# Kernel tuning notes

Hardware: AMD Instinct MI355X
Metric: run time of the kernel (lower is better)

Reference implementation:

```python
import jax, jax.numpy as jnp
import numpy as np

SEED_THRESHOLD = 0.5
DUPLICATE_THRESHOLD = 0.8


def setup_inputs() -> dict:
    key = jax.random.key(0)
    k1, k2 = jax.random.split(key)
    B, Q, C = 16, 1800, 256
    return {
        "query_signatures": jax.random.normal(k1, (B, Q, C), dtype=jnp.float32),
        "query_seed_logits": jax.random.normal(k2, (B, Q), dtype=jnp.float32),
    }


def _cc_labels(adj):
    """Connected-component labels via min-label propagation. adj: [Q,Q] bool (symmetric).
    Label of each node = smallest node index in its component. Unconnected nodes keep own index."""
    Q = adj.shape[0]
    labels0 = jnp.arange(Q, dtype=jnp.int32)

    def cond(state):
        return state[1]

    def body(state):
        labels, _ = state
        nbr_min = jnp.min(jnp.where(adj, labels[None, :], Q), axis=1)
        new = jnp.minimum(labels, nbr_min)
        return new, jnp.any(new != labels)

    labels, _ = jax.lax.while_loop(cond, body, (labels0, jnp.bool_(True)))
    return labels


def reference(query_signatures, query_seed_logits):
    sig = query_signatures                     # [B,Q,C]
    B, Q, C = sig.shape
    qidx = jnp.arange(Q)

    scores = jax.nn.sigmoid(query_seed_logits.astype(jnp.float32))   # [B,Q]
    selected = scores >= SEED_THRESHOLD                               # [B,Q]
    # fallback: if no query selected in an image, select the argmax-score query
    empty = ~jnp.any(selected, axis=1)                                # [B]
    fb = jnp.argmax(scores, axis=1)                                   # [B]
    selected = selected | (empty[:, None] & (qidx[None, :] == fb[:, None]))

    # cosine pairwise similarity
    nrm = jnp.linalg.norm(sig, axis=-1, keepdims=True)
    nsig = sig / jnp.maximum(nrm, 1e-12)
    sim = jnp.einsum("bqc,bkc->bqk", nsig, nsig)                      # [B,Q,Q]

    adj = (sim >= DUPLICATE_THRESHOLD) & selected[:, :, None] & selected[:, None, :]
    adj = adj.at[:, qidx, qidx].set(selected)                         # diag = selected

    labels = jax.vmap(_cc_labels)(adj)                                # [B,Q] int32

    # a label slot l hosts a component iff node l is selected and is its own component min
    active = selected & (labels == qidx[None, :].astype(labels.dtype))  # [B,Q]

    # per-component best-score member (components visited in ascending min-index order,
    # matching the torch BFS-from-ascending-node order)
    member = (labels[:, None, :] == qidx[None, :, None].astype(labels.dtype)) & selected[:, None, :]  # [B,Ql,Qn]
    masked_scores = jnp.where(member, scores[:, None, :], -jnp.inf)
    best = jnp.argmax(masked_scores, axis=2)                          # [B,Q] node index of best per label
    best_sig = jnp.take_along_axis(sig, best[..., None], axis=1)      # [B,Q,C]
    best_score = jnp.take_along_axis(scores, best, axis=1)            # [B,Q]

    # compact active components to the front (pad to Q, the static max)
    pos = jnp.cumsum(active, axis=1) - 1
    dest = jnp.where(active, pos, Q)                                  # inactive -> dropped

    seed_signatures = jax.vmap(
        lambda d, v: jnp.zeros((Q, C), sig.dtype).at[d].set(v, mode="drop")
    )(dest, best_sig)
    seed_scores = jax.vmap(
        lambda d, v: jnp.zeros((Q,), scores.dtype).at[d].set(v, mode="drop")
    )(dest, best_score)

    num_seeds = jnp.sum(active, axis=1)
    pad_mask = qidx[None, :] < num_seeds[:, None]
    return seed_signatures, pad_mask, seed_scores
```

## Files before the change

### kernel.cpp

```cpp
#include <hip/hip_runtime.h>
#include <hip/hip_bf16.h>
#include <stdint.h>

#define B_ 16
#define Q_ 1800
#define C_ 256
#define WPR 29
#define QPAD 1856
#define TBK 15
#define OUT_SIG_ELEMS (B_*Q_*C_)

typedef unsigned long long u64;
typedef unsigned int u32;
typedef __attribute__((ext_vector_type(8))) short bf16x8;
typedef __attribute__((ext_vector_type(4))) float f32x4;

__global__ __launch_bounds__(256)
void k_compact(const float* __restrict__ logits, float* __restrict__ scores,
               int* __restrict__ sel_idx, int* __restrict__ sel_cnt) {
  int b = blockIdx.x, t = threadIdx.x;
  int lane = t & 63, wid = t >> 6;
  __shared__ int wsum[4];
  __shared__ int s_tot;
  __shared__ u64 kw[4];
  const float* lgb = logits + b * Q_;
  float* scb = scores + b * Q_;

  int f[8]; int cnt = 0; u64 mk = 0;
  #pragma unroll
  for (int e = 0; e < 8; ++e) {
    int q = t * 8 + e;
    int fl = 0;
    if (q < Q_) {
      float sc = 1.0f / (1.0f + expf(-lgb[q]));
      scb[q] = sc;
      fl = (sc >= 0.5f) ? 1 : 0;
      u64 key = ((u64)__float_as_uint(sc) << 32) | (u32)(~(u32)q);
      mk = (mk > key) ? mk : key;
    }
    f[e] = fl; cnt += fl;
  }

  int incl = cnt;
  #pragma unroll
  for (int d = 1; d < 64; d <<= 1) {
    int v = __shfl_up(incl, d, 64);
    if (lane >= d) incl += v;
  }
  if (lane == 63) wsum[wid] = incl;
  __syncthreads();
  if (t == 0) {
    int acc = 0;
    #pragma unroll
    for (int i = 0; i < 4; ++i) { int v = wsum[i]; wsum[i] = acc; acc += v; }
    s_tot = acc;
  }
  __syncthreads();
  int excl = wsum[wid] + incl - cnt;
  int total = s_tot;

  if (total > 0) {
    #pragma unroll
    for (int e = 0; e < 8; ++e) {
      if (f[e]) { sel_idx[b * Q_ + excl] = t * 8 + e; excl++; }
    }
    if (t == 0) sel_cnt[b] = total;
  } else {
    u64 r = mk;
    #pragma unroll
    for (int d = 1; d < 64; d <<= 1) {
      u64 o = __shfl_xor(r, d, 64);
      r = (o > r) ? o : r;
    }
    if (lane == 0) kw[wid] = r;
    __syncthreads();
    if (t == 0) {
      u64 m2 = kw[0];
      #pragma unroll
      for (int i = 1; i < 4; ++i) m2 = (kw[i] > m2) ? kw[i] : m2;
      sel_idx[b * Q_] = (int)(~(u32)m2);
      sel_cnt[b] = 1;
    }
  }
}

__global__ __launch_bounds__(256)
void k_prep(const float* __restrict__ sig, const int* __restrict__ sel_idx,
            const int* __restrict__ sel_cnt, unsigned short* __restrict__ nsig,
            u32* __restrict__ rowmin) {
  int b = blockIdx.y;
  int p = blockIdx.x * 4 + (threadIdx.x >> 6);
  int lane = threadIdx.x & 63;
  int S = sel_cnt[b];
  int Spad = (S + 63) & ~63;
  if (p >= Spad) return;
  if (lane == 0) rowmin[b * QPAD + p] = 0xFFFFFFFFu;
  unsigned short* dst = nsig + ((size_t)b * QPAD + p) * C_;
  if (p >= S) {
    *reinterpret_cast<uint2*>(dst + lane * 4) = make_uint2(0u, 0u);
    return;
  }
  int row = sel_idx[b * Q_ + p];
  const float* src = sig + ((size_t)b * Q_ + row) * C_;
  float4 v = *reinterpret_cast<const float4*>(src + lane * 4);
  float ss = v.x * v.x + v.y * v.y + v.z * v.z + v.w * v.w;
  #pragma unroll
  for (int m = 32; m; m >>= 1) ss += __shfl_xor(ss, m, 64);
  float inv = 1.0f / fmaxf(sqrtf(ss), 1e-12f);
  __hip_bfloat16 h0 = __float2bfloat16(v.x * inv);
  __hip_bfloat16 h1 = __float2bfloat16(v.y * inv);
  __hip_bfloat16 h2 = __float2bfloat16(v.z * inv);
  __hip_bfloat16 h3 = __float2bfloat16(v.w * inv);
  unsigned short u0, u1, u2, u3;
  __builtin_memcpy(&u0, &h0, 2); __builtin_memcpy(&u1, &h1, 2);
  __builtin_memcpy(&u2, &h2, 2); __builtin_memcpy(&u3, &h3, 2);
  uint2 wv;
  wv.x = (u32)u0 | ((u32)u1 << 16);
  wv.y = (u32)u2 | ((u32)u3 << 16);
  *reinterpret_cast<uint2*>(dst + lane * 4) = wv;
}

__global__ __launch_bounds__(256)
void k_sim(const unsigned short* __restrict__ nsig, const int* __restrict__ sel_cnt,
           u64* __restrict__ adj, u32* __restrict__ rowmin) {
  int lin = blockIdx.x;
  int b = lin & 15;
  int tile = lin >> 4;
  int tib = tile / TBK, tjb = tile - tib * TBK;
  if (tib > tjb) return;
  int S = sel_cnt[b];
  if (tjb * 128 >= S || tib * 128 >= S) return;
  const bool diag = (tib == tjb);

  __shared__ uint4 Alds[2048];
  __shared__ uint4 Blds[2048];
  __shared__ u64 adjtile[4][64];

  const int t = threadIdx.x;
  const int wv = t >> 6, lane = t & 63;
  const int lr = lane & 15, lg = lane >> 4;

  const int i1 = tib * 128 + (wv >> 1) * 64;
  const int j1 = tjb * 128 + (wv & 1) * 64;
  const bool live = (i1 < S) && (j1 < S);

  const char* gbase = (const char*)(nsig + (size_t)b * QPAD * C_);
  const char* arow = gbase + (size_t)tib * 128 * 512;
  const char* brow = gbase + (size_t)tjb * 128 * 512;

  f32x4 acc[4][4];
  #pragma unroll
  for (int rs = 0; rs < 4; ++rs)
    #pragma unroll
    for (int cg = 0; cg < 4; ++cg) acc[rs][cg] = (f32x4){0.f, 0.f, 0.f, 0.f};

  const int ra0 = (wv >> 1) * 64;
  const int rb0 = (wv & 1) * 64;
  const char* Bbase = reinterpret_cast<const char*>(diag ? Alds : Blds);

  for (int kh = 0; kh < 2; ++kh) {
    #pragma unroll
    for (int it = 0; it < 8; ++it) {
      int o = it * 4096 + t * 16;
      int r = o >> 8;
      int w = o & 255;
      int sw = o ^ ((r & 7) << 4);
      uint4 va = *reinterpret_cast<const uint4*>(arow + (size_t)r * 512 + kh * 256 + w);
      Alds[sw >> 4] = va;
      if (!diag) {
        uint4 vb = *reinterpret_cast<const uint4*>(brow + (size_t)r * 512 + kh * 256 + w);
        Blds[sw >> 4] = vb;
      }
    }
    __syncthreads();
    if (live) {
      #pragma unroll
      for (int ks = 0; ks < 4; ++ks) {
        bf16x8 af[4], bf[4];
        #pragma unroll
        for (int rs = 0; rs < 4; ++rs) {
          int r = ra0 + rs * 16 + lr;
          int byte = r * 256 + ((ks * 64 + lg * 16) ^ ((r & 7) << 4));
          af[rs] = *reinterpret_cast<const bf16x8*>(
              reinterpret_cast<const char*>(Alds) + byte);
        }
        #pragma unroll
        for (int cg = 0; cg < 4; ++cg) {
          int r = rb0 + cg * 16 + lr;
          int byte = r * 256 + ((ks * 64 + lg * 16) ^ ((r & 7) << 4));
          bf[cg] = *reinterpret_cast<const bf16x8*>(Bbase + byte);
        }
        #pragma unroll
        for (int rs = 0; rs < 4; ++rs)
          #pragma unroll
          for (int cg = 0; cg < 4; ++cg)
            acc[rs][cg] = __builtin_amdgcn_mfma_f32_16x16x32_bf16(
                af[rs], bf[cg], acc[rs][cg], 0, 0, 0);
      }
    }
    __syncthreads();
  }

  if (!live) return;
  adjtile[wv][lane] = 0ull;
  #pragma unroll
  for (int rs = 0; rs < 4; ++rs) {
    #pragma unroll
    for (int j = 0; j < 4; ++j) {
      u64 bits = 0ull;
      if (acc[rs][0][j] >= 0.8f) bits |= 1ull << (0  + lr);
      if (acc[rs][1][j] >= 0.8f) bits |= 1ull << (16 + lr);
      if (acc[rs][2][j] >= 0.8f) bits |= 1ull << (32 + lr);
      if (acc[rs][3][j] >= 0.8f) bits |= 1ull << (48 + lr);
      if (bits) atomicOr(&adjtile[wv][rs * 16 + lg * 4 + j], bits);
    }
  }
  int gi = i1 + lane;
  u64 word = adjtile[wv][lane];
  if (gi < S) {
    adj[((size_t)b * Q_ + gi) * WPR + (j1 >> 6)] = word;
    if (word) atomicMin(&rowmin[b * QPAD + gi], (u32)(j1 + __builtin_ctzll(word)));
  }

  if (!diag) {
    u64 tw = 0ull;
    for (int i = 0; i < 64; ++i)
      tw |= ((adjtile[wv][i] >> lane) & 1ull) << i;
    int gj = j1 + lane;
    if (gj < S) {
      adj[((size_t)b * Q_ + gj) * WPR + (i1 >> 6)] = tw;
      if (tw) atomicMin(&rowmin[b * QPAD + gj], (u32)(i1 + __builtin_ctzll(tw)));
    }
  }
}

__global__ __launch_bounds__(1024)
void k_cc(const float* __restrict__ scores, const int* __restrict__ sel_idx,
          const int* __restrict__ sel_cnt, const u64* __restrict__ adj,
          const u32* __restrict__ rowmin,
          int* __restrict__ best_idx, float* __restrict__ best_sc,
          int* __restrict__ nroots) {
  int b = blockIdx.x, t = threadIdx.x;
  int lane = t & 63, wid = t >> 6;
  __shared__ int lab[Q_];
  __shared__ int lab2[Q_];
  __shared__ u64 best[Q_];
  __shared__ int wsum[16];
  __shared__ int s_tot;
  __shared__ int s_changed;

  int S = sel_cnt[b];
  int nw = (S + 63) >> 6;
  const u64* arow0 = adj + (size_t)b * Q_ * WPR;

  if (t == 0) s_changed = 0;
  __syncthreads();
  for (int s = t; s < S; s += 1024) {
    u32 m = rowmin[b * QPAD + s];
    u32 v = ((u32)s < m) ? (u32)s : m;
    lab[s] = (int)v;
    if (v != (u32)s) s_changed = 1;
  }
  __syncthreads();

  if (s_changed) {
    for (int iter = 0; iter < Q_ + 2; ++iter) {
      if (t == 0) s_changed = 0;
      __syncthreads();
      for (int s = t; s < S; s += 1024) {
        int m = lab[s];
        const u64* row = arow0 + (size_t)s * WPR;
        for (int w = 0; w < nw; ++w) {
          u64 msk = row[w];
          while (msk) {
            int j = (w << 6) + __builtin_ctzll(msk);
            int lj = lab[j];
            m = (lj < m) ? lj : m;
            msk &= msk - 1;
          }
        }
        lab2[s] = m;
        if (m != lab[s]) s_changed = 1;
      }
      __syncthreads();
      int ch = s_changed;
      for (int s = t; s < S; s += 1024) lab[s] = lab2[s];
      __syncthreads();
      if (!ch) break;
    }
  }

  for (int s = t; s < S; s += 1024) best[s] = 0ull;
  __syncthreads();
  const float* scb = scores + b * Q_;
  const int* sidx = sel_idx + b * Q_;
  for (int s = t; s < S; s += 1024) {
    int orig = sidx[s];
    float sc = scb[orig];
    u64 key = ((u64)__float_as_uint(sc) << 32) | (u32)(~(u32)orig);
    atomicMax(&best[lab[s]], key);
  }
  __syncthreads();

  int f[2]; int cnt = 0;
  #pragma unroll
  for (int e = 0; e < 2; ++e) {
    int s = t * 2 + e;
    int fl = (s < S && lab[s] == s) ? 1 : 0;
    f[e] = fl; cnt += fl;
  }
  int incl = cnt;
  #pragma unroll
  for (int d = 1; d < 64; d <<= 1) {
    int v = __shfl_up(incl, d, 64);
    if (lane >= d) incl += v;
  }
  if (lane == 63) wsum[wid] = incl;
  __syncthreads();
  if (t == 0) {
    int acc = 0;
    #pragma unroll
    for (int i = 0; i < 16; ++i) { int v = wsum[i]; wsum[i] = acc; acc += v; }
    s_tot = acc;
  }
  __syncthreads();
  int excl = wsum[wid] + incl - cnt;
  #pragma unroll
  for (int e = 0; e < 2; ++e) {
    if (f[e]) {
      int s = t * 2 + e;
      u64 key = best[s];
      best_idx[b * Q_ + excl] = (int)(~(u32)key);
      best_sc[b * Q_ + excl] = __uint_as_float((u32)(key >> 32));
      excl++;
    }
  }
  if (t == 0) nroots[b] = s_tot;
}

__global__ __launch_bounds__(256)
void k_gather(const float* __restrict__ sig, const int* __restrict__ best_idx,
              const float* __restrict__ best_sc, const int* __restrict__ nroots,
              float* __restrict__ out_sig, float* __restrict__ out_mask,
              float* __restrict__ out_scores) {
  int b = blockIdx.y;
  int p = blockIdx.x * 4 + (threadIdx.x >> 6);
  int lane = threadIdx.x & 63;
  if (p >= Q_) return;
  int n = nroots[b];
  float* orow = out_sig + ((size_t)b * Q_ + p) * C_;
  if (p < n) {
    int row = best_idx[b * Q_ + p];
    float4 v = *reinterpret_cast<const float4*>(sig + ((size_t)b * Q_ + row) * C_ + lane * 4);
    *reinterpret_cast<float4*>(orow + lane * 4) = v;
    if (lane == 0) {
      out_mask[b * Q_ + p] = 1.0f;
      out_scores[b * Q_ + p] = best_sc[b * Q_ + p];
    }
  } else {
    *reinterpret_cast<float4*>(orow + lane * 4) = make_float4(0.f, 0.f, 0.f, 0.f);
    if (lane == 0) {
      out_mask[b * Q_ + p] = 0.0f;
      out_scores[b * Q_ + p] = 0.0f;
    }
  }
}

extern "C" void kernel_launch(void* const* d_in, const int* in_sizes, int n_in,
                              void* d_out, int out_size, void* d_ws, size_t ws_size,
                              hipStream_t stream) {
  const float* p0 = (const float*)d_in[0];
  const float* p1 = (const float*)d_in[1];
  const float* sig;  const float* logits;
  if (in_sizes[0] == B_ * Q_ * C_) { sig = p0; logits = p1; }
  else                             { sig = p1; logits = p0; }

  float* out = (float*)d_out;
  float* out_mask   = out + OUT_SIG_ELEMS;
  float* out_scores = out + OUT_SIG_ELEMS + B_ * Q_;

  char* ws = (char*)d_ws;
  float* scores  = (float*)ws;  ws += B_ * Q_ * 4;
  int* sel_idx   = (int*)ws;    ws += B_ * Q_ * 4;
  int* best_idx  = (int*)ws;    ws += B_ * Q_ * 4;
  float* best_sc = (float*)ws;  ws += B_ * Q_ * 4;
  int* sel_cnt   = (int*)ws;    ws += 256;
  int* nroots    = (int*)ws;    ws += 256;

  u64* adj = (u64*)d_out;
  unsigned short* nsig = (unsigned short*)((char*)d_out + (size_t)(8u << 20));
  u32* rowmin = (u32*)((char*)d_out + (size_t)(26u << 20));

  k_compact<<<B_, 256, 0, stream>>>(logits, scores, sel_idx, sel_cnt);

  dim3 gp(QPAD / 4, B_);
  k_prep<<<gp, 256, 0, stream>>>(sig, sel_idx, sel_cnt, nsig, rowmin);

  k_sim<<<B_ * TBK * TBK, 256, 0, stream>>>(nsig, sel_cnt, adj, rowmin);

  k_cc<<<B_, 1024, 0, stream>>>(scores, sel_idx, sel_cnt, adj, rowmin,
                                best_idx, best_sc, nroots);

  dim3 gg(Q_ / 4, B_);
  k_gather<<<gg, 256, 0, stream>>>(sig, best_idx, best_sc, nroots,
                                   out, out_mask, out_scores);
}
```

Measured before the change: 45.20 us.

## Fuse compaction into prep, triangular sim grid, and merge CC with gather

Each prep block now recomputes the sigmoid, prefix-sum compaction and fallback itself, so the separate compaction kernel and its launch go away. The similarity grid launches only upper-triangular tiles instead of returning early from lower ones. When the workspace is large enough, adjacency and rowmin move into the workspace. A new fused kernel then has every gather block redundantly recompute the selection, the component labels and the best member before writing its four output rows. This removes two launches and the global round-trips of intermediate buffers, but repeats the per-batch label propagation and best-score work in every gather block, which gets costly if many components need iterations.

```diff
diff --git a/kernel.cpp b/kernel.cpp
--- a/kernel.cpp
+++ b/kernel.cpp
@@ -8,6 +8,7 @@
 #define WPR 29
 #define QPAD 1856
 #define TBK 15
+#define NTRI 120
 #define OUT_SIG_ELEMS (B_*Q_*C_)
 
 typedef unsigned long long u64;
@@ -16,37 +17,32 @@
 typedef __attribute__((ext_vector_type(4))) float f32x4;
 
 __global__ __launch_bounds__(256)
-void k_compact(const float* __restrict__ logits, float* __restrict__ scores,
-               int* __restrict__ sel_idx, int* __restrict__ sel_cnt) {
-  int b = blockIdx.x, t = threadIdx.x;
-  int lane = t & 63, wid = t >> 6;
+void k_prep2(const float* __restrict__ sig, const float* __restrict__ logits,
+             int* __restrict__ sel_idx, int* __restrict__ sel_cnt,
+             unsigned short* __restrict__ nsig, u32* __restrict__ rowmin) {
+  const int b = blockIdx.y, g = blockIdx.x;
+  const int t = threadIdx.x, lane = t & 63, wid = t >> 6;
   __shared__ int wsum[4];
+  __shared__ u64 kw[4];
   __shared__ int s_tot;
-  __shared__ u64 kw[4];
+  __shared__ int slot[4];
+
   const float* lgb = logits + b * Q_;
-  float* scb = scores + b * Q_;
-
   int f[8]; int cnt = 0; u64 mk = 0;
   #pragma unroll
   for (int e = 0; e < 8; ++e) {
-    int q = t * 8 + e;
-    int fl = 0;
+    int q = t * 8 + e; int fl = 0;
     if (q < Q_) {
       float sc = 1.0f / (1.0f + expf(-lgb[q]));
-      scb[q] = sc;
       fl = (sc >= 0.5f) ? 1 : 0;
       u64 key = ((u64)__float_as_uint(sc) << 32) | (u32)(~(u32)q);
       mk = (mk > key) ? mk : key;
     }
     f[e] = fl; cnt += fl;
   }
-
   int incl = cnt;
   #pragma unroll
-  for (int d = 1; d < 64; d <<= 1) {
-    int v = __shfl_up(incl, d, 64);
-    if (lane >= d) incl += v;
-  }
+  for (int d = 1; d < 64; d <<= 1) { int v = __shfl_up(incl, d, 64); if (lane >= d) incl += v; }
   if (lane == 63) wsum[wid] = incl;
   __syncthreads();
   if (t == 0) {
@@ -56,43 +52,45 @@
     s_tot = acc;
   }
   __syncthreads();
-  int excl = wsum[wid] + incl - cnt;
-  int total = s_tot;
-
-  if (total > 0) {
-    #pragma unroll
-    for (int e = 0; e < 8; ++e) {
-      if (f[e]) { sel_idx[b * Q_ + excl] = t * 8 + e; excl++; }
-    }
-    if (t == 0) sel_cnt[b] = total;
-  } else {
+  int excl0 = wsum[wid] + incl - cnt;
+  int S = s_tot;
+  int fbq = -1;
+  if (S == 0) {
     u64 r = mk;
     #pragma unroll
-    for (int d = 1; d < 64; d <<= 1) {
-      u64 o = __shfl_xor(r, d, 64);
-      r = (o > r) ? o : r;
-    }
+    for (int d = 1; d < 64; d <<= 1) { u64 o = __shfl_xor(r, d, 64); r = (o > r) ? o : r; }
     if (lane == 0) kw[wid] = r;
     __syncthreads();
-    if (t == 0) {
-      u64 m2 = kw[0];
-      #pragma unroll
-      for (int i = 1; i < 4; ++i) m2 = (kw[i] > m2) ? kw[i] : m2;
-      sel_idx[b * Q_] = (int)(~(u32)m2);
-      sel_cnt[b] = 1;
-    }
-  }
-}
-
-__global__ __launch_bounds__(256)
-void k_prep(const float* __restrict__ sig, const int* __restrict__ sel_idx,
-            const int* __restrict__ sel_cnt, unsigned short* __restrict__ nsig,
-            u32* __restrict__ rowmin) {
-  int b = blockIdx.y;
-  int p = blockIdx.x * 4 + (threadIdx.x >> 6);
-  int lane = threadIdx.x & 63;
-  int S = sel_cnt[b];
+    u64 m2 = kw[0];
+    #pragma unroll
+    for (int i = 1; i < 4; ++i) m2 = (kw[i] > m2) ? kw[i] : m2;
+    fbq = (int)(~(u32)m2);
+    S = 1;
+  }
+  if (g == 0 && t == 0) sel_cnt[b] = S;
+
   int Spad = (S + 63) & ~63;
+  if (g * 4 >= Spad) return;
+
+  if (t < 4) slot[t] = -1;
+  __syncthreads();
+  if (fbq >= 0) {
+    if (g == 0 && t == 0) { slot[0] = fbq; sel_idx[b * Q_] = fbq; }
+  } else {
+    int ex = excl0;
+    #pragma unroll
+    for (int e = 0; e < 8; ++e) {
+      if (f[e]) {
+        int q = t * 8 + e;
+        if (g == 0) sel_idx[b * Q_ + ex] = q;
+        if (ex >= g * 4 && ex < g * 4 + 4) slot[ex - g * 4] = q;
+        ex++;
+      }
+    }
+  }
+  __syncthreads();
+
+  int p = g * 4 + wid;
   if (p >= Spad) return;
   if (lane == 0) rowmin[b * QPAD + p] = 0xFFFFFFFFu;
   unsigned short* dst = nsig + ((size_t)b * QPAD + p) * C_;
@@ -100,7 +98,7 @@
     *reinterpret_cast<uint2*>(dst + lane * 4) = make_uint2(0u, 0u);
     return;
   }
-  int row = sel_idx[b * Q_ + p];
+  int row = slot[wid];
   const float* src = sig + ((size_t)b * Q_ + row) * C_;
   float4 v = *reinterpret_cast<const float4*>(src + lane * 4);
   float ss = v.x * v.x + v.y * v.y + v.z * v.z + v.w * v.w;
@@ -125,11 +123,11 @@
            u64* __restrict__ adj, u32* __restrict__ rowmin) {
   int lin = blockIdx.x;
   int b = lin & 15;
-  int tile = lin >> 4;
-  int tib = tile / TBK, tjb = tile - tib * TBK;
-  if (tib > tjb) return;
+  int u = lin >> 4, tib = 0;
+  while (u >= TBK - tib) { u -= TBK - tib; ++tib; }
+  int tjb = tib + u;
   int S = sel_cnt[b];
-  if (tjb * 128 >= S || tib * 128 >= S) return;
+  if (tjb * 128 >= S) return;
   const bool diag = (tib == tjb);
 
   __shared__ uint4 Alds[2048];
@@ -221,7 +219,6 @@
     adj[((size_t)b * Q_ + gi) * WPR + (j1 >> 6)] = word;
     if (word) atomicMin(&rowmin[b * QPAD + gi], (u32)(j1 + __builtin_ctzll(word)));
   }
-
   if (!diag) {
     u64 tw = 0ull;
     for (int i = 0; i < 64; ++i)
@@ -234,12 +231,187 @@
   }
 }
 
+__global__ __launch_bounds__(256)
+void k_ccgather(const float* __restrict__ sig, const float* __restrict__ logits,
+                const u32* __restrict__ rowmin, const u64* __restrict__ adj,
+                float* __restrict__ out_sig, float* __restrict__ out_mask,
+                float* __restrict__ out_scores) {
+  const int b = blockIdx.y, g = blockIdx.x;
+  const int t = threadIdx.x, lane = t & 63, wid = t >> 6;
+  __shared__ int lab[Q_];
+  __shared__ int lab2[Q_];
+  __shared__ u64 best[Q_];
+  __shared__ int wsum[4];
+  __shared__ u64 kw[4];
+  __shared__ int s_tot;
+  __shared__ int s_chg;
+  __shared__ int slot[4];
+
+  const float* lgb = logits + b * Q_;
+  int f[8]; float sv[8]; int cnt = 0; u64 mk = 0;
+  #pragma unroll
+  for (int e = 0; e < 8; ++e) {
+    int q = t * 8 + e; int fl = 0; float sc = 0.f;
+    if (q < Q_) {
+      sc = 1.0f / (1.0f + expf(-lgb[q]));
+      fl = (sc >= 0.5f) ? 1 : 0;
+      u64 key = ((u64)__float_as_uint(sc) << 32) | (u32)(~(u32)q);
+      mk = (mk > key) ? mk : key;
+    }
+    f[e] = fl; sv[e] = sc; cnt += fl;
+  }
+  int incl = cnt;
+  #pragma unroll
+  for (int d = 1; d < 64; d <<= 1) { int v = __shfl_up(incl, d, 64); if (lane >= d) incl += v; }
+  if (lane == 63) wsum[wid] = incl;
+  if (t == 0) s_chg = 0;
+  __syncthreads();
+  if (t == 0) {
+    int acc = 0;
+    #pragma unroll
+    for (int i = 0; i < 4; ++i) { int v = wsum[i]; wsum[i] = acc; acc += v; }
+    s_tot = acc;
+  }
+  __syncthreads();
+  int excl0 = wsum[wid] + incl - cnt;
+  int S = s_tot;
+  int fbq = -1;
+  if (S == 0) {
+    u64 r = mk;
+    #pragma unroll
+    for (int d = 1; d < 64; d <<= 1) { u64 o = __shfl_xor(r, d, 64); r = (o > r) ? o : r; }
+    if (lane == 0) kw[wid] = r;
+    __syncthreads();
+    u64 m2 = kw[0];
+    #pragma unroll
+    for (int i = 1; i < 4; ++i) m2 = (kw[i] > m2) ? kw[i] : m2;
+    fbq = (int)(~(u32)m2);
+    S = 1;
+  }
+
+  for (int s = t; s < S; s += 256) best[s] = 0ull;
+  if (fbq >= 0) {
+    if (t == 0) lab[0] = 0;
+  } else {
+    int ex = excl0;
+    #pragma unroll
+    for (int e = 0; e < 8; ++e) {
+      if (f[e]) {
+        u32 m = rowmin[b * QPAD + ex];
+        u32 v = ((u32)ex < m) ? (u32)ex : m;
+        lab[ex] = (int)v;
+        if (v != (u32)ex) s_chg = 1;
+        ex++;
+      }
+    }
+  }
+  __syncthreads();
+
+  if (s_chg) {
+    const u64* arow0 = adj + (size_t)b * Q_ * WPR;
+    int nw = (S + 63) >> 6;
+    for (int iter = 0; iter < Q_ + 2; ++iter) {
+      if (t == 0) s_chg = 0;
+      __syncthreads();
+      for (int s = t; s < S; s += 256) {
+        int m = lab[s];
+        const u64* row = arow0 + (size_t)s * WPR;
+        for (int w = 0; w < nw; ++w) {
+          u64 msk = row[w];
+          while (msk) {
+            int j = (w << 6) + __builtin_ctzll(msk);
+            int lj = lab[j];
+            m = (lj < m) ? lj : m;
+            msk &= msk - 1;
+          }
+        }
+        lab2[s] = m;
+        if (m != lab[s]) s_chg = 1;
+      }
+      __syncthreads();
+      int ch = s_chg;
+      for (int s = t; s < S; s += 256) lab[s] = lab2[s];
+      __syncthreads();
+      if (!ch) break;
+    }
+  }
+
+  if (fbq >= 0) {
+    if (t == 0) {
+      float sc = 1.0f / (1.0f + expf(-lgb[fbq]));
+      best[0] = ((u64)__float_as_uint(sc) << 32) | (u32)(~(u32)fbq);
+    }
+  } else {
+    int ex = excl0;
+    #pragma unroll
+    for (int e = 0; e < 8; ++e) {
+      if (f[e]) {
+        int q = t * 8 + e;
+        u64 key = ((u64)__float_as_uint(sv[e]) << 32) | (u32)(~(u32)q);
+        atomicMax(&best[lab[ex]], key);
+        ex++;
+      }
+    }
+  }
+  __syncthreads();
+
+  int rf[8]; int rcnt = 0;
+  #pragma unroll
+  for (int e = 0; e < 8; ++e) {
+    int s = t * 8 + e;
+    int fl = (s < S && lab[s] == s) ? 1 : 0;
+    rf[e] = fl; rcnt += fl;
+  }
+  int rincl = rcnt;
+  #pragma unroll
+  for (int d = 1; d < 64; d <<= 1) { int v = __shfl_up(rincl, d, 64); if (lane >= d) rincl += v; }
+  if (t < 4) slot[t] = -1;
+  if (lane == 63) wsum[wid] = rincl;
+  __syncthreads();
+  if (t == 0) {
+    int acc = 0;
+    #pragma unroll
+    for (int i = 0; i < 4; ++i) { int v = wsum[i]; wsum[i] = acc; acc += v; }
+    s_tot = acc;
+  }
+  __syncthreads();
+  int rex = wsum[wid] + rincl - rcnt;
+  #pragma unroll
+  for (int e = 0; e < 8; ++e) {
+    if (rf[e]) {
+      if (rex >= g * 4 && rex < g * 4 + 4) slot[rex - g * 4] = t * 8 + e;
+      rex++;
+    }
+  }
+  __syncthreads();
+  int n = s_tot;
+
+  int p = g * 4 + wid;
+  float* orow = out_sig + ((size_t)b * Q_ + p) * C_;
+  if (p < n) {
+    u64 key = best[slot[wid]];
+    int orig = (int)(~(u32)key);
+    float4 v = *reinterpret_cast<const float4*>(sig + ((size_t)b * Q_ + orig) * C_ + lane * 4);
+    *reinterpret_cast<float4*>(orow + lane * 4) = v;
+    if (lane == 0) {
+      out_mask[b * Q_ + p] = 1.0f;
+      out_scores[b * Q_ + p] = __uint_as_float((u32)(key >> 32));
+    }
+  } else {
+    *reinterpret_cast<float4*>(orow + lane * 4) = make_float4(0.f, 0.f, 0.f, 0.f);
+    if (lane == 0) {
+      out_mask[b * Q_ + p] = 0.0f;
+      out_scores[b * Q_ + p] = 0.0f;
+    }
+  }
+}
+
 __global__ __launch_bounds__(1024)
-void k_cc(const float* __restrict__ scores, const int* __restrict__ sel_idx,
-          const int* __restrict__ sel_cnt, const u64* __restrict__ adj,
-          const u32* __restrict__ rowmin,
-          int* __restrict__ best_idx, float* __restrict__ best_sc,
-          int* __restrict__ nroots) {
+void k_cc2(const float* __restrict__ logits, const int* __restrict__ sel_idx,
+           const int* __restrict__ sel_cnt, const u64* __restrict__ adj,
+           const u32* __restrict__ rowmin,
+           int* __restrict__ best_idx, float* __restrict__ best_sc,
+           int* __restrict__ nroots) {
   int b = blockIdx.x, t = threadIdx.x;
   int lane = t & 63, wid = t >> 6;
   __shared__ int lab[Q_];
@@ -292,11 +464,10 @@
 
   for (int s = t; s < S; s += 1024) best[s] = 0ull;
   __syncthreads();
-  const float* scb = scores + b * Q_;
   const int* sidx = sel_idx + b * Q_;
   for (int s = t; s < S; s += 1024) {
     int orig = sidx[s];
-    float sc = scb[orig];
+    float sc = 1.0f / (1.0f + expf(-logits[b * Q_ + orig]));
     u64 key = ((u64)__float_as_uint(sc) << 32) | (u32)(~(u32)orig);
     atomicMax(&best[lab[s]], key);
   }
@@ -379,29 +550,37 @@
   float* out_mask   = out + OUT_SIG_ELEMS;
   float* out_scores = out + OUT_SIG_ELEMS + B_ * Q_;
 
-  char* ws = (char*)d_ws;
-  float* scores  = (float*)ws;  ws += B_ * Q_ * 4;
-  int* sel_idx   = (int*)ws;    ws += B_ * Q_ * 4;
-  int* best_idx  = (int*)ws;    ws += B_ * Q_ * 4;
-  float* best_sc = (float*)ws;  ws += B_ * Q_ * 4;
-  int* sel_cnt   = (int*)ws;    ws += 256;
-  int* nroots    = (int*)ws;    ws += 256;
-
-  u64* adj = (u64*)d_out;
+  char* w = (char*)d_ws;
+  int* sel_cnt = (int*)w;  w += 256;
+  int* sel_idx = (int*)w;  w += B_ * Q_ * 4;
+
   unsigned short* nsig = (unsigned short*)((char*)d_out + (size_t)(8u << 20));
-  u32* rowmin = (u32*)((char*)d_out + (size_t)(26u << 20));
-
-  k_compact<<<B_, 256, 0, stream>>>(logits, scores, sel_idx, sel_cnt);
-
+
+  const size_t need_big = 256 + (size_t)B_ * Q_ * 4 +
+                          (size_t)B_ * QPAD * 4 + (size_t)B_ * Q_ * WPR * 8;
   dim3 gp(QPAD / 4, B_);
-  k_prep<<<gp, 256, 0, stream>>>(sig, sel_idx, sel_cnt, nsig, rowmin);
-
-  k_sim<<<B_ * TBK * TBK, 256, 0, stream>>>(nsig, sel_cnt, adj, rowmin);
-
-  k_cc<<<B_, 1024, 0, stream>>>(scores, sel_idx, sel_cnt, adj, rowmin,
-                                best_idx, best_sc, nroots);
-
   dim3 gg(Q_ / 4, B_);
-  k_gather<<<gg, 256, 0, stream>>>(sig, best_idx, best_sc, nroots,
-                                   out, out_mask, out_scores);
+
+  if (ws_size >= need_big) {
+    u32* rowmin = (u32*)w;  w += (size_t)B_ * QPAD * 4;
+    u64* adj    = (u64*)w;
+
+    k_prep2<<<gp, 256, 0, stream>>>(sig, logits, sel_idx, sel_cnt, nsig, rowmin);
+    k_sim<<<B_ * NTRI, 256, 0, stream>>>(nsig, sel_cnt, adj, rowmin);
+    k_ccgather<<<gg, 256, 0, stream>>>(sig, logits, rowmin, adj,
+                                       out, out_mask, out_scores);
+  } else {
+    int* best_idx  = (int*)w;   w += B_ * Q_ * 4;
+    float* best_sc = (float*)w; w += B_ * Q_ * 4;
+    int* nroots    = (int*)w;   w += 256;
+    u64* adj    = (u64*)d_out;
+    u32* rowmin = (u32*)((char*)d_out + (size_t)(26u << 20));
+
+    k_prep2<<<gp, 256, 0, stream>>>(sig, logits, sel_idx, sel_cnt, nsig, rowmin);
+    k_sim<<<B_ * NTRI, 256, 0, stream>>>(nsig, sel_cnt, adj, rowmin);
+    k_cc2<<<B_, 1024, 0, stream>>>(logits, sel_idx, sel_cnt, adj, rowmin,
+                                   best_idx, best_sc, nroots);
+    k_gather<<<gg, 256, 0, stream>>>(sig, best_idx, best_sc, nroots,
+                                     out, out_mask, out_scores);
+  }
 }
```

Result: slower. 99.81 us (+120.8%).
